# Kernel tuning notes

Hardware: AMD Instinct MI355X
Metric: run time of the kernel (lower is better)

## Reference

```python
import jax, jax.numpy as jnp
import numpy as np

KNN = 10       # knn_size
TOPK = 4       # top_k_select
H = 4          # num_heads
HID = 64       # edge-MLP hidden dim


def setup_inputs() -> dict:
    key = jax.random.key(0)
    ks = jax.random.split(key, 12)
    B, V, D = 4, 4096, 256
    s = 0.02
    return {
        "voxel_tokens": jax.random.normal(ks[0], (B, V, D), jnp.float32),
        "voxel_coords": jax.random.uniform(ks[1], (B, V, 3), jnp.float32) * 10.0,
        "mask": jnp.ones((B, V), dtype=bool),
        # EdgeScoringMLP: Linear(2D+3 -> 64), Linear(64 -> 1)
        "W1": jax.random.normal(ks[2], (2 * D + 3, HID), jnp.float32) * s,
        "b1": jnp.zeros((HID,), jnp.float32),
        "W2": jax.random.normal(ks[3], (HID, 1), jnp.float32) * s,
        "b2": jnp.zeros((1,), jnp.float32),
        # CrossAttention projections (D -> D)
        "Wq": jax.random.normal(ks[4], (D, D), jnp.float32) * s,
        "bq": jnp.zeros((D,), jnp.float32),
        "Wk": jax.random.normal(ks[5], (D, D), jnp.float32) * s,
        "bk": jnp.zeros((D,), jnp.float32),
        "Wv": jax.random.normal(ks[6], (D, D), jnp.float32) * s,
        "bv": jnp.zeros((D,), jnp.float32),
        "Wo": jax.random.normal(ks[7], (D, D), jnp.float32) * s,
        "bo": jnp.zeros((D,), jnp.float32),
    }


def reference(voxel_tokens, voxel_coords, mask,
              W1, b1, W2, b2, Wq, bq, Wk, bk, Wv, bv, Wo, bo):
    # mask is all-True (Vp == V per batch element), so the original per-batch
    # loop over dynamic voxel counts is an exact vmap over B. Dropouts are in
    # eval mode (identity).
    D = voxel_tokens.shape[-1]
    Dh = D // H

    def single(tok, coo):  # tok: (V, D), coo: (V, 3)
        # --- KNN graph build (squared euclidean; monotonic in true cdist) ---
        sq = jnp.sum(coo * coo, axis=-1)                        # (V,)
        d2 = sq[:, None] + sq[None, :] - 2.0 * (coo @ coo.T)    # (V, V)
        _, knn = jax.lax.top_k(-d2, KNN + 1)                    # smallest dists
        knn = knn[:, 1:]                                        # drop self, (V, KNN)

        # --- edge features: [anchor_tok, neighbor_tok, rel_pos] ---
        nb_tok = tok[knn]                                       # (V, KNN, D)
        rel = coo[knn] - coo[:, None, :]                        # (V, KNN, 3)
        anchor = jnp.broadcast_to(tok[:, None, :], nb_tok.shape)
        ef = jnp.concatenate([anchor, nb_tok, rel], axis=-1)    # (V, KNN, 2D+3)

        # --- edge-MLP scoring + softmax + top-k edge select ---
        sc = (jax.nn.relu(ef @ W1 + b1) @ W2 + b2)[..., 0]      # (V, KNN)
        aw = jax.nn.softmax(sc, axis=-1)
        _, loc = jax.lax.top_k(aw, TOPK)                        # (V, TOPK)
        sel = jnp.take_along_axis(knn, loc, axis=-1)            # (V, TOPK)
        nbr = tok[sel]                                          # (V, TOPK, D)

        # --- cross attention over selected neighbors ---
        Q = (tok @ Wq + bq).reshape(-1, H, Dh)                  # (V, H, Dh)
        K = (nbr @ Wk + bk).reshape(-1, TOPK, H, Dh)            # (V, TOPK, H, Dh)
        Vv = (nbr @ Wv + bv).reshape(-1, TOPK, H, Dh)
        att = jnp.einsum('vhd,vshd->vhs', Q, K) / jnp.sqrt(jnp.float32(Dh))
        w = jax.nn.softmax(att, axis=-1)                        # (V, H, TOPK)
        out = jnp.einsum('vhs,vshd->vhd', w, Vv).reshape(-1, D)
        return out @ Wo + bo                                    # (V, D)

    return jax.vmap(single)(voxel_tokens, voxel_coords)        # (B, V, D)
```

## Files before the change

### kernel.cpp

```cpp
#include <hip/hip_runtime.h>
#include <hip/hip_bf16.h>

#define VV 4096
#define DDIM 256
#define KNN_K 10
#define TK 4

__device__ __forceinline__ float f_sq3(float x, float y, float z) {
    return __fadd_rn(__fadd_rn(__fmul_rn(x, x), __fmul_rn(y, y)), __fmul_rn(z, z));
}
__device__ __forceinline__ float f_dot3(float ax, float ay, float az,
                                        float bx, float by, float bz) {
    float d = __fmul_rn(ax, bx);
    d = __fmaf_rn(ay, by, d);
    d = __fmaf_rn(az, bz, d);
    return d;
}

__device__ __forceinline__ unsigned long long mkkey(float d2, int j) {
    unsigned u = __float_as_uint(d2);
    u ^= (unsigned)((int)u >> 31) | 0x80000000u;
    return ((unsigned long long)u << 32) | (unsigned)j;
}

__device__ __forceinline__ void fma44(const float4 a, const float4 b, float (&c)[4][4]) {
    c[0][0] = fmaf(a.x, b.x, c[0][0]); c[0][1] = fmaf(a.x, b.y, c[0][1]);
    c[0][2] = fmaf(a.x, b.z, c[0][2]); c[0][3] = fmaf(a.x, b.w, c[0][3]);
    c[1][0] = fmaf(a.y, b.x, c[1][0]); c[1][1] = fmaf(a.y, b.y, c[1][1]);
    c[1][2] = fmaf(a.y, b.z, c[1][2]); c[1][3] = fmaf(a.y, b.w, c[1][3]);
    c[2][0] = fmaf(a.z, b.x, c[2][0]); c[2][1] = fmaf(a.z, b.y, c[2][1]);
    c[2][2] = fmaf(a.z, b.z, c[2][2]); c[2][3] = fmaf(a.z, b.w, c[2][3]);
    c[3][0] = fmaf(a.w, b.x, c[3][0]); c[3][1] = fmaf(a.w, b.y, c[3][1]);
    c[3][2] = fmaf(a.w, b.z, c[3][2]); c[3][3] = fmaf(a.w, b.w, c[3][3]);
}

__global__ void __launch_bounds__(256) an_gemm_kernel(
    const float* __restrict__ tok,
    const float* __restrict__ W1,
    const float* __restrict__ coords,
    float* __restrict__ AN,
    float4* __restrict__ cxyzs)
{
    __shared__ float As[16][68];
    __shared__ float Bs[16][68];

    const int mBlock = blockIdx.x * 64;
    const int grp    = blockIdx.y;
    const float* W   = W1 + (size_t)grp * 256 * 64;

    const int tid = threadIdx.x;

    if (grp == 0 && tid < 64) {
        int m = mBlock + tid;
        float x = coords[m * 3 + 0], y = coords[m * 3 + 1], z = coords[m * 3 + 2];
        cxyzs[m] = make_float4(x, y, z, f_sq3(x, y, z));
    }

    const int tx = tid & 15;
    const int ty = tid >> 4;

    const int ar  = tid >> 2;
    const int ac4 = tid & 3;
    const int br  = tid >> 4;
    const int bc4 = tid & 15;

    float acc[4][4] = {};

    for (int k0 = 0; k0 < 256; k0 += 16) {
        float4 a4 = *(const float4*)&tok[(size_t)(mBlock + ar) * 256 + k0 + ac4 * 4];
        As[ac4 * 4 + 0][ar] = a4.x;
        As[ac4 * 4 + 1][ar] = a4.y;
        As[ac4 * 4 + 2][ar] = a4.z;
        As[ac4 * 4 + 3][ar] = a4.w;
        float4 b4 = *(const float4*)&W[(size_t)(k0 + br) * 64 + bc4 * 4];
        *(float4*)&Bs[br][bc4 * 4] = b4;
        __syncthreads();
        #pragma unroll
        for (int kk = 0; kk < 16; kk++) {
            float4 av = *(const float4*)&As[kk][ty * 4];
            float4 bv4 = *(const float4*)&Bs[kk][tx * 4];
            fma44(av, bv4, acc);
        }
        __syncthreads();
    }

    #pragma unroll
    for (int i = 0; i < 4; i++) {
        int m = mBlock + ty * 4 + i;
        float4 o;
        o.x = acc[i][0]; o.y = acc[i][1]; o.z = acc[i][2]; o.w = acc[i][3];
        *(float4*)&AN[(size_t)m * 128 + grp * 64 + tx * 4] = o;
    }
}

__global__ void __launch_bounds__(256) knn_score_kernel(
    const float* __restrict__ AN,
    const float4* __restrict__ cxyzs,
    const float* __restrict__ W1,
    const float* __restrict__ b1,
    const float* __restrict__ W2,
    int* __restrict__ sel)
{
    const int tid  = threadIdx.x;
    const int lane = tid & 63;
    const int wave = tid >> 6;
    const int q    = blockIdx.x * 4 + wave;
    const int base = q & ~4095;
    const int v    = q & 4095;
    const float4* cx = cxyzs + base;

    __shared__ int   sKnn[4][KNN_K];
    __shared__ float sSc[4][KNN_K];
    __shared__ float sHid[4][KNN_K][65];

    float4 cq = cx[v];
    const float qx = cq.x, qy = cq.y, qz = cq.z, sqq = cq.w;

    unsigned long long best   = ~0ull;
    unsigned long long second = ~0ull;
    unsigned long long used   = 0ull;

    #pragma unroll 4
    for (int i = 0; i < 64; i++) {
        int j = i * 64 + lane;
        float4 c = cx[j];
        float dt  = f_dot3(qx, qy, qz, c.x, c.y, c.z);
        float d2v = __fsub_rn(__fadd_rn(sqq, c.w), __fmul_rn(2.0f, dt));
        unsigned long long k = mkkey(d2v, j);
        if (k < best) { second = best; best = k; }
        else if (k < second) { second = k; }
    }

    #pragma unroll 1
    for (int it = 0; it < 11; it++) {
        unsigned long long rb = best;
        #pragma unroll
        for (int off = 1; off < 64; off <<= 1) {
            unsigned olo = __shfl_xor((unsigned)rb, off);
            unsigned ohi = __shfl_xor((unsigned)(rb >> 32), off);
            unsigned long long o = ((unsigned long long)ohi << 32) | olo;
            if (o < rb) rb = o;
        }
        int wj = (int)((unsigned)rb & 4095u);
        if (it >= 1 && lane == 0) sKnn[wave][it - 1] = wj;

        if ((unsigned)best == (unsigned)rb) {
            used |= 1ull << (wj >> 6);
            best = second;
            second = ~0ull;
            if (best == ~0ull) {
                #pragma unroll 1
                for (int i = 0; i < 64; i++) {
                    if ((used >> i) & 1ull) continue;
                    int j = i * 64 + lane;
                    float4 c = cx[j];
                    float dt  = f_dot3(qx, qy, qz, c.x, c.y, c.z);
                    float d2v = __fsub_rn(__fadd_rn(sqq, c.w), __fmul_rn(2.0f, dt));
                    unsigned long long k = mkkey(d2v, j);
                    if (k < best) { second = best; best = k; }
                    else if (k < second) { second = k; }
                }
            }
        }
    }

    const float sAl = AN[(size_t)q * 128 + lane];
    const float b1l = b1[lane];
    const float wr0 = W1[(512 + 0) * 64 + lane];
    const float wr1 = W1[(512 + 1) * 64 + lane];
    const float wr2 = W1[(512 + 2) * 64 + lane];

    #pragma unroll 1
    for (int nb = 0; nb < KNN_K; nb++) {
        int kn = sKnn[wave][nb];
        float4 cn = cx[kn];
        float acc = __fadd_rn(sAl, AN[(size_t)(base + kn) * 128 + 64 + lane]);
        float rel0 = __fsub_rn(cn.x, qx);
        acc = __fmaf_rn(rel0, wr0, acc);
        float rel1 = __fsub_rn(cn.y, qy);
        acc = __fmaf_rn(rel1, wr1, acc);
        float rel2 = __fsub_rn(cn.z, qz);
        acc = __fmaf_rn(rel2, wr2, acc);
        float hid = __fadd_rn(acc, b1l);
        sHid[wave][nb][lane] = hid > 0.0f ? hid : 0.0f;
    }

    if (lane < KNN_K) {
        float s = 0.0f;
        #pragma unroll 8
        for (int h = 0; h < 64; h++)
            s = __fmaf_rn(sHid[wave][lane][h], W2[h], s);
        sSc[wave][lane] = s;
    }

    if (lane == 0) {
        unsigned um = 0;
        #pragma unroll
        for (int s = 0; s < TK; s++) {
            float bests = -3.4e38f; int bj = 0;
            for (int jj = 0; jj < KNN_K; jj++) {
                if (um & (1u << jj)) continue;
                float sc = sSc[wave][jj];
                if (sc > bests) { bests = sc; bj = jj; }
            }
            um |= 1u << bj;
            sel[(size_t)q * TK + s] = base + sKnn[wave][bj];
        }
    }
}

__global__ void __launch_bounds__(256, 1) qkv_gemm_kernel(
    const float* __restrict__ tok,
    const float* __restrict__ Wq, const float* __restrict__ bq,
    const float* __restrict__ Wk, const float* __restrict__ bk,
    const float* __restrict__ Wv, const float* __restrict__ bv,
    float* __restrict__ qkv)
{
    __shared__ float As[16][132];
    __shared__ float Bs[16][132];

    const int mBlock = blockIdx.x * 128;
    const int nb     = blockIdx.y;
    const int grp    = nb >> 1;
    const int nIn    = (nb & 1) * 128;
    const float* W    = (grp == 0) ? Wq : (grp == 1) ? Wk : Wv;
    const float* bias = (grp == 0) ? bq : (grp == 1) ? bk : bv;

    const int tid = threadIdx.x;
    const int tx = tid & 15;
    const int ty = tid >> 4;
    const int ar  = tid >> 2;
    const int ac4 = tid & 3;
    const int br  = tid >> 4;
    const int bc4 = tid & 15;

    float acc00[4][4] = {}, acc01[4][4] = {}, acc10[4][4] = {}, acc11[4][4] = {};

    for (int k0 = 0; k0 < 256; k0 += 16) {
        float4 a0 = *(const float4*)&tok[(size_t)(mBlock + ar) * 256 + k0 + ac4 * 4];
        float4 a1 = *(const float4*)&tok[(size_t)(mBlock + 64 + ar) * 256 + k0 + ac4 * 4];
        As[ac4 * 4 + 0][ar] = a0.x;      As[ac4 * 4 + 0][64 + ar] = a1.x;
        As[ac4 * 4 + 1][ar] = a0.y;      As[ac4 * 4 + 1][64 + ar] = a1.y;
        As[ac4 * 4 + 2][ar] = a0.z;      As[ac4 * 4 + 2][64 + ar] = a1.z;
        As[ac4 * 4 + 3][ar] = a0.w;      As[ac4 * 4 + 3][64 + ar] = a1.w;
        float4 b0 = *(const float4*)&W[(size_t)(k0 + br) * 256 + nIn + bc4 * 4];
        float4 b1v = *(const float4*)&W[(size_t)(k0 + br) * 256 + nIn + 64 + bc4 * 4];
        *(float4*)&Bs[br][bc4 * 4] = b0;
        *(float4*)&Bs[br][64 + bc4 * 4] = b1v;
        __syncthreads();
        #pragma unroll
        for (int kk = 0; kk < 16; kk++) {
            float4 av0 = *(const float4*)&As[kk][ty * 4];
            float4 av1 = *(const float4*)&As[kk][64 + ty * 4];
            float4 bv0 = *(const float4*)&Bs[kk][tx * 4];
            float4 bv1 = *(const float4*)&Bs[kk][64 + tx * 4];
            fma44(av0, bv0, acc00);
            fma44(av0, bv1, acc01);
            fma44(av1, bv0, acc10);
            fma44(av1, bv1, acc11);
        }
        __syncthreads();
    }

    #pragma unroll
    for (int i = 0; i < 4; i++) {
        int m0 = mBlock + ty * 4 + i;
        int m1 = m0 + 64;
        int c0 = nIn + tx * 4;
        int c1 = c0 + 64;
        float4 o;
        o.x = acc00[i][0] + bias[c0 + 0]; o.y = acc00[i][1] + bias[c0 + 1];
        o.z = acc00[i][2] + bias[c0 + 2]; o.w = acc00[i][3] + bias[c0 + 3];
        *(float4*)&qkv[(size_t)m0 * 768 + grp * 256 + c0] = o;
        o.x = acc01[i][0] + bias[c1 + 0]; o.y = acc01[i][1] + bias[c1 + 1];
        o.z = acc01[i][2] + bias[c1 + 2]; o.w = acc01[i][3] + bias[c1 + 3];
        *(float4*)&qkv[(size_t)m0 * 768 + grp * 256 + c1] = o;
        o.x = acc10[i][0] + bias[c0 + 0]; o.y = acc10[i][1] + bias[c0 + 1];
        o.z = acc10[i][2] + bias[c0 + 2]; o.w = acc10[i][3] + bias[c0 + 3];
        *(float4*)&qkv[(size_t)m1 * 768 + grp * 256 + c0] = o;
        o.x = acc11[i][0] + bias[c1 + 0]; o.y = acc11[i][1] + bias[c1 + 1];
        o.z = acc11[i][2] + bias[c1 + 2]; o.w = acc11[i][3] + bias[c1 + 3];
        *(float4*)&qkv[(size_t)m1 * 768 + grp * 256 + c1] = o;
    }
}

__global__ void __launch_bounds__(256) attn_gather_kernel(
    const float* __restrict__ qkv, const int* __restrict__ sel,
    float* __restrict__ attnout)
{
    const int tid  = threadIdx.x;
    const int lane = tid & 63;
    const int wave = tid >> 6;
    const int q    = blockIdx.x * 4 + wave;

    int rows[TK];
    #pragma unroll
    for (int s = 0; s < TK; s++) rows[s] = sel[(size_t)q * TK + s];

    const float* qrow = qkv + (size_t)q * 768;

    #pragma unroll
    for (int h = 0; h < 4; h++) {
        const int d = h * 64 + lane;
        const float qv = qrow[d];

        float att[TK];
        #pragma unroll
        for (int s = 0; s < TK; s++) {
            float p = qv * qkv[(size_t)rows[s] * 768 + 256 + d];
            #pragma unroll
            for (int m = 1; m < 64; m <<= 1) p += __shfl_xor(p, m);
            att[s] = p * 0.125f;
        }

        float mx  = fmaxf(fmaxf(att[0], att[1]), fmaxf(att[2], att[3]));
        float e0 = expf(att[0] - mx), e1 = expf(att[1] - mx),
              e2 = expf(att[2] - mx), e3 = expf(att[3] - mx);
        float inv = 1.0f / (e0 + e1 + e2 + e3);

        float o = (e0 * qkv[(size_t)rows[0] * 768 + 512 + d] +
                   e1 * qkv[(size_t)rows[1] * 768 + 512 + d] +
                   e2 * qkv[(size_t)rows[2] * 768 + 512 + d] +
                   e3 * qkv[(size_t)rows[3] * 768 + 512 + d]) * inv;

        attnout[(size_t)q * 256 + d] = o;
    }
}

__global__ void __launch_bounds__(256, 1) wo_gemm_kernel(
    const float* __restrict__ A,
    const float* __restrict__ Wo, const float* __restrict__ bo,
    float* __restrict__ out)
{
    __shared__ float As[16][132];
    __shared__ float Bs[16][132];

    const int mBlock = blockIdx.x * 128;
    const int nBlock = blockIdx.y * 128;

    const int tid = threadIdx.x;
    const int tx = tid & 15;
    const int ty = tid >> 4;
    const int ar  = tid >> 2;
    const int ac4 = tid & 3;
    const int br  = tid >> 4;
    const int bc4 = tid & 15;

    float acc00[4][4] = {}, acc01[4][4] = {}, acc10[4][4] = {}, acc11[4][4] = {};

    for (int k0 = 0; k0 < 256; k0 += 16) {
        float4 a0 = *(const float4*)&A[(size_t)(mBlock + ar) * 256 + k0 + ac4 * 4];
        float4 a1 = *(const float4*)&A[(size_t)(mBlock + 64 + ar) * 256 + k0 + ac4 * 4];
        As[ac4 * 4 + 0][ar] = a0.x;      As[ac4 * 4 + 0][64 + ar] = a1.x;
        As[ac4 * 4 + 1][ar] = a0.y;      As[ac4 * 4 + 1][64 + ar] = a1.y;
        As[ac4 * 4 + 2][ar] = a0.z;      As[ac4 * 4 + 2][64 + ar] = a1.z;
        As[ac4 * 4 + 3][ar] = a0.w;      As[ac4 * 4 + 3][64 + ar] = a1.w;
        float4 b0 = *(const float4*)&Wo[(size_t)(k0 + br) * 256 + nBlock + bc4 * 4];
        float4 b1v = *(const float4*)&Wo[(size_t)(k0 + br) * 256 + nBlock + 64 + bc4 * 4];
        *(float4*)&Bs[br][bc4 * 4] = b0;
        *(float4*)&Bs[br][64 + bc4 * 4] = b1v;
        __syncthreads();
        #pragma unroll
        for (int kk = 0; kk < 16; kk++) {
            float4 av0 = *(const float4*)&As[kk][ty * 4];
            float4 av1 = *(const float4*)&As[kk][64 + ty * 4];
            float4 bv0 = *(const float4*)&Bs[kk][tx * 4];
            float4 bv1 = *(const float4*)&Bs[kk][64 + tx * 4];
            fma44(av0, bv0, acc00);
            fma44(av0, bv1, acc01);
            fma44(av1, bv0, acc10);
            fma44(av1, bv1, acc11);
        }
        __syncthreads();
    }

    #pragma unroll
    for (int i = 0; i < 4; i++) {
        int m0 = mBlock + ty * 4 + i;
        int m1 = m0 + 64;
        int c0 = nBlock + tx * 4;
        int c1 = c0 + 64;
        float4 o;
        o.x = acc00[i][0] + bo[c0 + 0]; o.y = acc00[i][1] + bo[c0 + 1];
        o.z = acc00[i][2] + bo[c0 + 2]; o.w = acc00[i][3] + bo[c0 + 3];
        *(float4*)&out[(size_t)m0 * 256 + c0] = o;
        o.x = acc01[i][0] + bo[c1 + 0]; o.y = acc01[i][1] + bo[c1 + 1];
        o.z = acc01[i][2] + bo[c1 + 2]; o.w = acc01[i][3] + bo[c1 + 3];
        *(float4*)&out[(size_t)m0 * 256 + c1] = o;
        o.x = acc10[i][0] + bo[c0 + 0]; o.y = acc10[i][1] + bo[c0 + 1];
        o.z = acc10[i][2] + bo[c0 + 2]; o.w = acc10[i][3] + bo[c0 + 3];
        *(float4*)&out[(size_t)m1 * 256 + c0] = o;
        o.x = acc11[i][0] + bo[c1 + 0]; o.y = acc11[i][1] + bo[c1 + 1];
        o.z = acc11[i][2] + bo[c1 + 2]; o.w = acc11[i][3] + bo[c1 + 3];
        *(float4*)&out[(size_t)m1 * 256 + c1] = o;
    }
}

__global__ void __launch_bounds__(256) fused_voxel_attn(
    const float* __restrict__ tok,
    const float* __restrict__ coords,
    const float* __restrict__ W1,
    const float* __restrict__ b1,
    const float* __restrict__ W2,
    const float* __restrict__ Wq, const float* __restrict__ bq,
    const float* __restrict__ Wk, const float* __restrict__ bk,
    const float* __restrict__ Wv, const float* __restrict__ bv,
    const float* __restrict__ Wo, const float* __restrict__ bo,
    float* __restrict__ out, int out_size)
{
    const int q    = blockIdx.x;
    const int b    = q >> 12;
    const int v    = q & 4095;
    const int base = q & ~4095;
    const int tid  = threadIdx.x;
    const float* cb = coords + (size_t)b * VV * 3;

    __shared__ float  sval[256];
    __shared__ int    sidx[256];
    __shared__ int    sKnn[KNN_K];
    __shared__ int    sSel[TK];
    __shared__ float  sTokA[DDIM];
    __shared__ float  sTokN[KNN_K][DDIM];
    __shared__ float  sAH[64];
    __shared__ float  sHid[KNN_K][64];
    __shared__ float  sSc[KNN_K];
    __shared__ float  sP[TK][256];
    __shared__ float  sAtt[4][TK];
    __shared__ float  sO[DDIM];

    const float qx = cb[v * 3 + 0];
    const float qy = cb[v * 3 + 1];
    const float qz = cb[v * 3 + 2];
    const float sqq = f_sq3(qx, qy, qz);

    float d2[16];
// ... 57 lines not shown
            acc = __fmaf_rn(tn[k], W1[(256 + k) * 64 + h], acc);
        #pragma unroll
        for (int c = 0; c < 3; c++) {
            float rel = __fsub_rn(cb[sKnn[nb] * 3 + c], cb[v * 3 + c]);
            acc = __fmaf_rn(rel, W1[(512 + c) * 64 + h], acc);
        }
        float hid = __fadd_rn(acc, b1[h]);
        sHid[nb][h] = hid > 0.0f ? hid : 0.0f;
    }
    __syncthreads();

    if (tid < KNN_K) {
        float s = 0.0f;
        for (int h = 0; h < 64; h++)
            s = __fmaf_rn(sHid[tid][h], W2[h], s);
        sSc[tid] = s;
    }
    __syncthreads();

    if (tid == 0) {
        unsigned um = 0;
        #pragma unroll
        for (int s = 0; s < TK; s++) {
            float best = -3.4e38f; int bj = 0;
            for (int jj = 0; jj < KNN_K; jj++) {
                if (um & (1u << jj)) continue;
                if (sSc[jj] > best) { best = sSc[jj]; bj = jj; }
            }
            um |= 1u << bj;
            sSel[s] = bj;
        }
    }
    __syncthreads();

    int ss[TK];
    float k_acc[TK], v_acc[TK];
    #pragma unroll
    for (int s = 0; s < TK; s++) {
        ss[s] = sSel[s];
        k_acc[s] = bk[tid];
        v_acc[s] = bv[tid];
    }
    float q_acc = bq[tid];

    for (int k = 0; k < 256; k++) {
        float wq = Wq[k * 256 + tid];
        float wk = Wk[k * 256 + tid];
        float wv = Wv[k * 256 + tid];
        q_acc += sTokA[k] * wq;
        #pragma unroll
        for (int s = 0; s < TK; s++) {
            float x = sTokN[ss[s]][k];
            k_acc[s] += x * wk;
            v_acc[s] += x * wv;
        }
    }

    #pragma unroll
    for (int s = 0; s < TK; s++) sP[s][tid] = q_acc * k_acc[s];
    __syncthreads();

    if (tid < 16) {
        int h = tid >> 2, s = tid & 3;
        float p = 0.0f;
        for (int d = 0; d < 64; d++) p += sP[s][h * 64 + d];
        sAtt[h][s] = p * 0.125f;
    }
    __syncthreads();

    const int hh = tid >> 6;
    float a0 = sAtt[hh][0], a1 = sAtt[hh][1], a2 = sAtt[hh][2], a3 = sAtt[hh][3];
    float mx  = fmaxf(fmaxf(a0, a1), fmaxf(a2, a3));
    float e0 = expf(a0 - mx), e1 = expf(a1 - mx), e2 = expf(a2 - mx), e3 = expf(a3 - mx);
    float inv = 1.0f / (e0 + e1 + e2 + e3);
    float o = (e0 * v_acc[0] + e1 * v_acc[1] + e2 * v_acc[2] + e3 * v_acc[3]) * inv;

    sO[tid] = o;
    __syncthreads();

    float a = bo[tid];
    for (int e = 0; e < 256; e++) a += sO[e] * Wo[e * 256 + tid];
    int oidx = q * DDIM + tid;
    if (oidx < out_size)
        out[oidx] = a;
}

extern "C" void kernel_launch(void* const* d_in, const int* in_sizes, int n_in,
                              void* d_out, int out_size, void* d_ws, size_t ws_size,
                              hipStream_t stream)
{
    const long long want[13] = {4194304LL, 49152LL, 32960LL, 64LL, 64LL,
                                65536LL, 256LL, 65536LL, 256LL,
                                65536LL, 256LL, 65536LL, 256LL};
    int idx[13];
    const int n = n_in;

    const long long* s64 = (const long long*)(const void*)in_sizes;
    const int*       s32 = in_sizes;

    bool ok = false;

    if (n >= 13 && s64[0] == want[0]) {
        ok = true;
        int walk = 0;
        for (int t = 0; t < 13; t++) {
            int f = -1;
            for (int i = walk; i < n; i++) {
                if (s64[i] == want[t]) { f = i; break; }
            }
            if (f < 0) { ok = false; break; }
            idx[t] = f; walk = f + 1;
        }
    }

    if (!ok) {
        ok = true;
        int walk = 0;
        for (int t = 0; t < 13; t++) {
            int f = -1;
            for (int i = walk; i < n; i++) {
                if ((long long)s32[i] == want[t]) { f = i; break; }
            }
            if (f < 0) { ok = false; break; }
            idx[t] = f; walk = f + 1;
        }
    }

    if (!ok) return;

    const float* tok    = (const float*)d_in[idx[0]];
    const float* coords = (const float*)d_in[idx[1]];
    const float* W1     = (const float*)d_in[idx[2]];
    const float* b1     = (const float*)d_in[idx[3]];
    const float* W2     = (const float*)d_in[idx[4]];
    const float* Wq     = (const float*)d_in[idx[5]];
    const float* bq     = (const float*)d_in[idx[6]];
    const float* Wk     = (const float*)d_in[idx[7]];
    const float* bk     = (const float*)d_in[idx[8]];
    const float* Wv     = (const float*)d_in[idx[9]];
    const float* bv     = (const float*)d_in[idx[10]];
    const float* Wo     = (const float*)d_in[idx[11]];
    const float* bo     = (const float*)d_in[idx[12]];
    float* out = (float*)d_out;

    const size_t NEED = 67633152;
    if (ws_size >= NEED) {
        char* ws = (char*)d_ws;
        int*    sel     = (int*)   (ws + 0);
        float*  AN      = (float*) (ws + 262144);
        float*  attnout = (float*) (ws + 262144);
        float*  qkv     = (float*) (ws + 17039360);
        float4* cxyzs   = (float4*)(ws + 67371008);

        an_gemm_kernel<<<dim3(256, 2), dim3(256), 0, stream>>>(tok, W1, coords, AN, cxyzs);
        knn_score_kernel<<<dim3(4096), dim3(256), 0, stream>>>(AN, cxyzs, W1, b1, W2, sel);
        qkv_gemm_kernel<<<dim3(128, 6), dim3(256), 0, stream>>>(tok, Wq, bq, Wk, bk, Wv, bv, qkv);
        attn_gather_kernel<<<dim3(4096), dim3(256), 0, stream>>>(qkv, sel, attnout);
        wo_gemm_kernel<<<dim3(128, 2), dim3(256), 0, stream>>>(attnout, Wo, bo, out);
    } else {
        fused_voxel_attn<<<dim3(16384), dim3(256), 0, stream>>>(
            tok, coords, W1, b1, W2, Wq, bq, Wk, bk, Wv, bv, Wo, bo, out, out_size);
    }
}
```

Baseline: 367.2 us.

## Fuse KNN scoring and QKV GEMM into one interleaved launch

New measurement: 376.1 us. 2.4% more time.

```diff
diff --git a/kernel.cpp b/kernel.cpp
--- a/kernel.cpp
+++ b/kernel.cpp
@@ -93,194 +93,199 @@
     }
 }
 
-__global__ void __launch_bounds__(256) knn_score_kernel(
+__global__ void __launch_bounds__(256, 1) knn_qkv_kernel(
     const float* __restrict__ AN,
     const float4* __restrict__ cxyzs,
     const float* __restrict__ W1,
     const float* __restrict__ b1,
     const float* __restrict__ W2,
-    int* __restrict__ sel)
-{
-    const int tid  = threadIdx.x;
-    const int lane = tid & 63;
-    const int wave = tid >> 6;
-    const int q    = blockIdx.x * 4 + wave;
-    const int base = q & ~4095;
-    const int v    = q & 4095;
-    const float4* cx = cxyzs + base;
-
-    __shared__ int   sKnn[4][KNN_K];
-    __shared__ float sSc[4][KNN_K];
-    __shared__ float sHid[4][KNN_K][65];
-
-    float4 cq = cx[v];
-    const float qx = cq.x, qy = cq.y, qz = cq.z, sqq = cq.w;
-
-    unsigned long long best   = ~0ull;
-    unsigned long long second = ~0ull;
-    unsigned long long used   = 0ull;
-
-    #pragma unroll 4
-    for (int i = 0; i < 64; i++) {
-        int j = i * 64 + lane;
-        float4 c = cx[j];
-        float dt  = f_dot3(qx, qy, qz, c.x, c.y, c.z);
-        float d2v = __fsub_rn(__fadd_rn(sqq, c.w), __fmul_rn(2.0f, dt));
-        unsigned long long k = mkkey(d2v, j);
-        if (k < best) { second = best; best = k; }
-        else if (k < second) { second = k; }
-    }
-
-    #pragma unroll 1
-    for (int it = 0; it < 11; it++) {
-        unsigned long long rb = best;
-        #pragma unroll
-        for (int off = 1; off < 64; off <<= 1) {
-            unsigned olo = __shfl_xor((unsigned)rb, off);
-            unsigned ohi = __shfl_xor((unsigned)(rb >> 32), off);
-            unsigned long long o = ((unsigned long long)ohi << 32) | olo;
-            if (o < rb) rb = o;
-        }
-        int wj = (int)((unsigned)rb & 4095u);
-        if (it >= 1 && lane == 0) sKnn[wave][it - 1] = wj;
-
-        if ((unsigned)best == (unsigned)rb) {
-            used |= 1ull << (wj >> 6);
-            best = second;
-            second = ~0ull;
-            if (best == ~0ull) {
-                #pragma unroll 1
-                for (int i = 0; i < 64; i++) {
-                    if ((used >> i) & 1ull) continue;
-                    int j = i * 64 + lane;
-                    float4 c = cx[j];
-                    float dt  = f_dot3(qx, qy, qz, c.x, c.y, c.z);
-                    float d2v = __fsub_rn(__fadd_rn(sqq, c.w), __fmul_rn(2.0f, dt));
-                    unsigned long long k = mkkey(d2v, j);
-                    if (k < best) { second = best; best = k; }
-                    else if (k < second) { second = k; }
-                }
-            }
-        }
-    }
-
-    const float sAl = AN[(size_t)q * 128 + lane];
-    const float b1l = b1[lane];
-    const float wr0 = W1[(512 + 0) * 64 + lane];
-    const float wr1 = W1[(512 + 1) * 64 + lane];
-    const float wr2 = W1[(512 + 2) * 64 + lane];
-
-    #pragma unroll 1
-    for (int nb = 0; nb < KNN_K; nb++) {
-        int kn = sKnn[wave][nb];
-        float4 cn = cx[kn];
-        float acc = __fadd_rn(sAl, AN[(size_t)(base + kn) * 128 + 64 + lane]);
-        float rel0 = __fsub_rn(cn.x, qx);
-        acc = __fmaf_rn(rel0, wr0, acc);
-        float rel1 = __fsub_rn(cn.y, qy);
-        acc = __fmaf_rn(rel1, wr1, acc);
-        float rel2 = __fsub_rn(cn.z, qz);
-        acc = __fmaf_rn(rel2, wr2, acc);
-        float hid = __fadd_rn(acc, b1l);
-        sHid[wave][nb][lane] = hid > 0.0f ? hid : 0.0f;
-    }
-
-    if (lane < KNN_K) {
-        float s = 0.0f;
-        #pragma unroll 8
-        for (int h = 0; h < 64; h++)
-            s = __fmaf_rn(sHid[wave][lane][h], W2[h], s);
-        sSc[wave][lane] = s;
-    }
-
-    if (lane == 0) {
-        unsigned um = 0;
-        #pragma unroll
-        for (int s = 0; s < TK; s++) {
-            float bests = -3.4e38f; int bj = 0;
-            for (int jj = 0; jj < KNN_K; jj++) {
-                if (um & (1u << jj)) continue;
-                float sc = sSc[wave][jj];
-                if (sc > bests) { bests = sc; bj = jj; }
-            }
-            um |= 1u << bj;
-            sel[(size_t)q * TK + s] = base + sKnn[wave][bj];
-        }
-    }
-}
-
-__global__ void __launch_bounds__(256, 1) qkv_gemm_kernel(
+    int* __restrict__ sel,
     const float* __restrict__ tok,
     const float* __restrict__ Wq, const float* __restrict__ bq,
     const float* __restrict__ Wk, const float* __restrict__ bk,
     const float* __restrict__ Wv, const float* __restrict__ bv,
     float* __restrict__ qkv)
 {
-    __shared__ float As[16][132];
-    __shared__ float Bs[16][132];
-
-    const int mBlock = blockIdx.x * 128;
-    const int nb     = blockIdx.y;
-    const int grp    = nb >> 1;
-    const int nIn    = (nb & 1) * 128;
-    const float* W    = (grp == 0) ? Wq : (grp == 1) ? Wk : Wv;
-    const float* bias = (grp == 0) ? bq : (grp == 1) ? bk : bv;
-
-    const int tid = threadIdx.x;
-    const int tx = tid & 15;
-    const int ty = tid >> 4;
-    const int ar  = tid >> 2;
-    const int ac4 = tid & 3;
-    const int br  = tid >> 4;
-    const int bc4 = tid & 15;
-
-    float acc00[4][4] = {}, acc01[4][4] = {}, acc10[4][4] = {}, acc11[4][4] = {};
-
-    for (int k0 = 0; k0 < 256; k0 += 16) {
-        float4 a0 = *(const float4*)&tok[(size_t)(mBlock + ar) * 256 + k0 + ac4 * 4];
-        float4 a1 = *(const float4*)&tok[(size_t)(mBlock + 64 + ar) * 256 + k0 + ac4 * 4];
-        As[ac4 * 4 + 0][ar] = a0.x;      As[ac4 * 4 + 0][64 + ar] = a1.x;
-        As[ac4 * 4 + 1][ar] = a0.y;      As[ac4 * 4 + 1][64 + ar] = a1.y;
-        As[ac4 * 4 + 2][ar] = a0.z;      As[ac4 * 4 + 2][64 + ar] = a1.z;
-        As[ac4 * 4 + 3][ar] = a0.w;      As[ac4 * 4 + 3][64 + ar] = a1.w;
-        float4 b0 = *(const float4*)&W[(size_t)(k0 + br) * 256 + nIn + bc4 * 4];
-        float4 b1v = *(const float4*)&W[(size_t)(k0 + br) * 256 + nIn + 64 + bc4 * 4];
-        *(float4*)&Bs[br][bc4 * 4] = b0;
-        *(float4*)&Bs[br][64 + bc4 * 4] = b1v;
-        __syncthreads();
-        #pragma unroll
-        for (int kk = 0; kk < 16; kk++) {
-            float4 av0 = *(const float4*)&As[kk][ty * 4];
-            float4 av1 = *(const float4*)&As[kk][64 + ty * 4];
-            float4 bv0 = *(const float4*)&Bs[kk][tx * 4];
-            float4 bv1 = *(const float4*)&Bs[kk][64 + tx * 4];
-            fma44(av0, bv0, acc00);
-            fma44(av0, bv1, acc01);
-            fma44(av1, bv0, acc10);
-            fma44(av1, bv1, acc11);
-        }
-        __syncthreads();
-    }
-
-    #pragma unroll
-    for (int i = 0; i < 4; i++) {
-        int m0 = mBlock + ty * 4 + i;
-        int m1 = m0 + 64;
-        int c0 = nIn + tx * 4;
-        int c1 = c0 + 64;
-        float4 o;
-        o.x = acc00[i][0] + bias[c0 + 0]; o.y = acc00[i][1] + bias[c0 + 1];
-        o.z = acc00[i][2] + bias[c0 + 2]; o.w = acc00[i][3] + bias[c0 + 3];
-        *(float4*)&qkv[(size_t)m0 * 768 + grp * 256 + c0] = o;
-        o.x = acc01[i][0] + bias[c1 + 0]; o.y = acc01[i][1] + bias[c1 + 1];
-        o.z = acc01[i][2] + bias[c1 + 2]; o.w = acc01[i][3] + bias[c1 + 3];
-        *(float4*)&qkv[(size_t)m0 * 768 + grp * 256 + c1] = o;
-        o.x = acc10[i][0] + bias[c0 + 0]; o.y = acc10[i][1] + bias[c0 + 1];
-        o.z = acc10[i][2] + bias[c0 + 2]; o.w = acc10[i][3] + bias[c0 + 3];
-        *(float4*)&qkv[(size_t)m1 * 768 + grp * 256 + c0] = o;
-        o.x = acc11[i][0] + bias[c1 + 0]; o.y = acc11[i][1] + bias[c1 + 1];
-        o.z = acc11[i][2] + bias[c1 + 2]; o.w = acc11[i][3] + bias[c1 + 3];
-        *(float4*)&qkv[(size_t)m1 * 768 + grp * 256 + c1] = o;
+    __shared__ __align__(16) char smem[16896];
+    const int tid   = threadIdx.x;
+    const int g     = blockIdx.x;
+    const int group = g / 19;
+    const int rem   = g - group * 19;
+
+    if (rem < 16) {
+        const int kb   = group * 16 + rem;
+        const int lane = tid & 63;
+        const int wave = tid >> 6;
+        const int q    = kb * 4 + wave;
+        const int base = q & ~4095;
+        const int v    = q & 4095;
+        const float4* cx = cxyzs + base;
+
+        int*   sKnn = (int*)smem;
+        float* sSc  = (float*)(smem + 160);
+        float* sHid = (float*)(smem + 320);
+
+        float4 cq = cx[v];
+        const float qx = cq.x, qy = cq.y, qz = cq.z, sqq = cq.w;
+
+        unsigned long long best   = ~0ull;
+        unsigned long long second = ~0ull;
+        unsigned long long used   = 0ull;
+
+        #pragma unroll 4
+        for (int i = 0; i < 64; i++) {
+            int j = i * 64 + lane;
+            float4 c = cx[j];
+            float dt  = f_dot3(qx, qy, qz, c.x, c.y, c.z);
+            float d2v = __fsub_rn(__fadd_rn(sqq, c.w), __fmul_rn(2.0f, dt));
+            unsigned long long k = mkkey(d2v, j);
+            if (k < best) { second = best; best = k; }
+            else if (k < second) { second = k; }
+        }
+
+        #pragma unroll 1
+        for (int it = 0; it < 11; it++) {
+            unsigned long long rb = best;
+            #pragma unroll
+            for (int off = 1; off < 64; off <<= 1) {
+                unsigned olo = __shfl_xor((unsigned)rb, off);
+                unsigned ohi = __shfl_xor((unsigned)(rb >> 32), off);
+                unsigned long long o = ((unsigned long long)ohi << 32) | olo;
+                if (o < rb) rb = o;
+            }
+            int wj = (int)((unsigned)rb & 4095u);
+            if (it >= 1 && lane == 0) sKnn[wave * KNN_K + it - 1] = wj;
+
+            if ((unsigned)best == (unsigned)rb) {
+                used |= 1ull << (wj >> 6);
+                best = second;
+                second = ~0ull;
+                if (best == ~0ull) {
+                    #pragma unroll 1
+                    for (int i = 0; i < 64; i++) {
+                        if ((used >> i) & 1ull) continue;
+                        int j = i * 64 + lane;
+                        float4 c = cx[j];
+                        float dt  = f_dot3(qx, qy, qz, c.x, c.y, c.z);
+                        float d2v = __fsub_rn(__fadd_rn(sqq, c.w), __fmul_rn(2.0f, dt));
+                        unsigned long long k = mkkey(d2v, j);
+                        if (k < best) { second = best; best = k; }
+                        else if (k < second) { second = k; }
+                    }
+                }
+            }
+        }
+
+        const float sAl = AN[(size_t)q * 128 + lane];
+        const float b1l = b1[lane];
+        const float wr0 = W1[(512 + 0) * 64 + lane];
+        const float wr1 = W1[(512 + 1) * 64 + lane];
+        const float wr2 = W1[(512 + 2) * 64 + lane];
+
+        #pragma unroll 1
+        for (int nb = 0; nb < KNN_K; nb++) {
+            int kn = sKnn[wave * KNN_K + nb];
+            float4 cn = cx[kn];
+            float acc = __fadd_rn(sAl, AN[(size_t)(base + kn) * 128 + 64 + lane]);
+            float rel0 = __fsub_rn(cn.x, qx);
+            acc = __fmaf_rn(rel0, wr0, acc);
+            float rel1 = __fsub_rn(cn.y, qy);
+            acc = __fmaf_rn(rel1, wr1, acc);
+            float rel2 = __fsub_rn(cn.z, qz);
+            acc = __fmaf_rn(rel2, wr2, acc);
+            float hid = __fadd_rn(acc, b1l);
+            sHid[(wave * KNN_K + nb) * 65 + lane] = hid > 0.0f ? hid : 0.0f;
+        }
+
+        if (lane < KNN_K) {
+            float s = 0.0f;
+            #pragma unroll 8
+            for (int h = 0; h < 64; h++)
+                s = __fmaf_rn(sHid[(wave * KNN_K + lane) * 65 + h], W2[h], s);
+            sSc[wave * KNN_K + lane] = s;
+        }
+
+        if (lane == 0) {
+            unsigned um = 0;
+            #pragma unroll
+            for (int s = 0; s < TK; s++) {
+                float bests = -3.4e38f; int bj = 0;
+                for (int jj = 0; jj < KNN_K; jj++) {
+                    if (um & (1u << jj)) continue;
+                    float sc = sSc[wave * KNN_K + jj];
+                    if (sc > bests) { bests = sc; bj = jj; }
+                }
+                um |= 1u << bj;
+                sel[(size_t)q * TK + s] = base + sKnn[wave * KNN_K + bj];
+            }
+        }
+    } else {
+        float* As = (float*)smem;
+        float* Bs = (float*)smem + 16 * 132;
+
+        const int id     = group * 3 + (rem - 16);
+        const int mBlock = (id & 127) * 128;
+        const int nb     = id >> 7;
+        const int grp    = nb >> 1;
+        const int nIn    = (nb & 1) * 128;
+        const float* W    = (grp == 0) ? Wq : (grp == 1) ? Wk : Wv;
+        const float* bias = (grp == 0) ? bq : (grp == 1) ? bk : bv;
+
+        const int tx = tid & 15;
+        const int ty = tid >> 4;
+        const int ar  = tid >> 2;
+        const int ac4 = tid & 3;
+        const int br  = tid >> 4;
+        const int bc4 = tid & 15;
+
+        float acc00[4][4] = {}, acc01[4][4] = {}, acc10[4][4] = {}, acc11[4][4] = {};
+
+        for (int k0 = 0; k0 < 256; k0 += 16) {
+            float4 a0 = *(const float4*)&tok[(size_t)(mBlock + ar) * 256 + k0 + ac4 * 4];
+            float4 a1 = *(const float4*)&tok[(size_t)(mBlock + 64 + ar) * 256 + k0 + ac4 * 4];
+            As[(ac4 * 4 + 0) * 132 + ar] = a0.x;      As[(ac4 * 4 + 0) * 132 + 64 + ar] = a1.x;
+            As[(ac4 * 4 + 1) * 132 + ar] = a0.y;      As[(ac4 * 4 + 1) * 132 + 64 + ar] = a1.y;
+            As[(ac4 * 4 + 2) * 132 + ar] = a0.z;      As[(ac4 * 4 + 2) * 132 + 64 + ar] = a1.z;
+            As[(ac4 * 4 + 3) * 132 + ar] = a0.w;      As[(ac4 * 4 + 3) * 132 + 64 + ar] = a1.w;
+            float4 b0 = *(const float4*)&W[(size_t)(k0 + br) * 256 + nIn + bc4 * 4];
+            float4 b1v = *(const float4*)&W[(size_t)(k0 + br) * 256 + nIn + 64 + bc4 * 4];
+            *(float4*)&Bs[br * 132 + bc4 * 4] = b0;
+            *(float4*)&Bs[br * 132 + 64 + bc4 * 4] = b1v;
+            __syncthreads();
+            #pragma unroll
+            for (int kk = 0; kk < 16; kk++) {
+                float4 av0 = *(const float4*)&As[kk * 132 + ty * 4];
+                float4 av1 = *(const float4*)&As[kk * 132 + 64 + ty * 4];
+                float4 bv0 = *(const float4*)&Bs[kk * 132 + tx * 4];
+                float4 bv1 = *(const float4*)&Bs[kk * 132 + 64 + tx * 4];
+                fma44(av0, bv0, acc00);
+                fma44(av0, bv1, acc01);
+                fma44(av1, bv0, acc10);
+                fma44(av1, bv1, acc11);
+            }
+            __syncthreads();
+        }
+
+        #pragma unroll
+        for (int i = 0; i < 4; i++) {
+            int m0 = mBlock + ty * 4 + i;
+            int m1 = m0 + 64;
+            int c0 = nIn + tx * 4;
+            int c1 = c0 + 64;
+            float4 o;
+            o.x = acc00[i][0] + bias[c0 + 0]; o.y = acc00[i][1] + bias[c0 + 1];
+            o.z = acc00[i][2] + bias[c0 + 2]; o.w = acc00[i][3] + bias[c0 + 3];
+            *(float4*)&qkv[(size_t)m0 * 768 + grp * 256 + c0] = o;
+            o.x = acc01[i][0] + bias[c1 + 0]; o.y = acc01[i][1] + bias[c1 + 1];
+            o.z = acc01[i][2] + bias[c1 + 2]; o.w = acc01[i][3] + bias[c1 + 3];
+            *(float4*)&qkv[(size_t)m0 * 768 + grp * 256 + c1] = o;
+            o.x = acc10[i][0] + bias[c0 + 0]; o.y = acc10[i][1] + bias[c0 + 1];
+            o.z = acc10[i][2] + bias[c0 + 2]; o.w = acc10[i][3] + bias[c0 + 3];
+            *(float4*)&qkv[(size_t)m1 * 768 + grp * 256 + c0] = o;
+            o.x = acc11[i][0] + bias[c1 + 0]; o.y = acc11[i][1] + bias[c1 + 1];
+            o.z = acc11[i][2] + bias[c1 + 2]; o.w = acc11[i][3] + bias[c1 + 3];
+            *(float4*)&qkv[(size_t)m1 * 768 + grp * 256 + c1] = o;
+        }
     }
 }
 
@@ -645,8 +650,8 @@
         float4* cxyzs   = (float4*)(ws + 67371008);
 
         an_gemm_kernel<<<dim3(256, 2), dim3(256), 0, stream>>>(tok, W1, coords, AN, cxyzs);
-        knn_score_kernel<<<dim3(4096), dim3(256), 0, stream>>>(AN, cxyzs, W1, b1, W2, sel);
-        qkv_gemm_kernel<<<dim3(128, 6), dim3(256), 0, stream>>>(tok, Wq, bq, Wk, bk, Wv, bv, qkv);
+        knn_qkv_kernel<<<dim3(4864), dim3(256), 0, stream>>>(
+            AN, cxyzs, W1, b1, W2, sel, tok, Wq, bq, Wk, bk, Wv, bv, qkv);
         attn_gather_kernel<<<dim3(4096), dim3(256), 0, stream>>>(qkv, sel, attnout);
         wo_gemm_kernel<<<dim3(128, 2), dim3(256), 0, stream>>>(attnout, Wo, bo, out);
     } else {
```

## Merge QKV and edge-MLP GEMMs into one launch; process two queries per wave in KNN

Applied to the files above, without the earlier changes.

Result: slower. 431.3 us (+17.5%).

```diff
diff --git a/kernel.cpp b/kernel.cpp
--- a/kernel.cpp
+++ b/kernel.cpp
@@ -34,62 +34,114 @@
     c[3][2] = fmaf(a.w, b.z, c[3][2]); c[3][3] = fmaf(a.w, b.w, c[3][3]);
 }
 
-__global__ void __launch_bounds__(256) an_gemm_kernel(
+__global__ void __launch_bounds__(256, 1) qkv_an_gemm_kernel(
     const float* __restrict__ tok,
+    const float* __restrict__ Wq, const float* __restrict__ bq,
+    const float* __restrict__ Wk, const float* __restrict__ bk,
+    const float* __restrict__ Wv, const float* __restrict__ bv,
     const float* __restrict__ W1,
     const float* __restrict__ coords,
+    float* __restrict__ qkv,
     float* __restrict__ AN,
     float4* __restrict__ cxyzs)
 {
-    __shared__ float As[16][68];
-    __shared__ float Bs[16][68];
-
-    const int mBlock = blockIdx.x * 64;
-    const int grp    = blockIdx.y;
-    const float* W   = W1 + (size_t)grp * 256 * 64;
-
-    const int tid = threadIdx.x;
-
-    if (grp == 0 && tid < 64) {
+    __shared__ float As[16][132];
+    __shared__ float Bs[16][132];
+
+    const int mBlock = blockIdx.x * 128;
+    const int nb     = blockIdx.y;
+    const int tid    = threadIdx.x;
+
+    if (nb == 6 && tid < 128) {
         int m = mBlock + tid;
         float x = coords[m * 3 + 0], y = coords[m * 3 + 1], z = coords[m * 3 + 2];
         cxyzs[m] = make_float4(x, y, z, f_sq3(x, y, z));
     }
 
+    const int grp    = nb >> 1;
+    const int nIn    = (nb & 1) * 128;
+    const float* W    = (grp == 0) ? Wq : (grp == 1) ? Wk : Wv;
+    const float* bias = (grp == 0) ? bq : (grp == 1) ? bk : bv;
+
     const int tx = tid & 15;
     const int ty = tid >> 4;
-
     const int ar  = tid >> 2;
     const int ac4 = tid & 3;
     const int br  = tid >> 4;
     const int bc4 = tid & 15;
 
-    float acc[4][4] = {};
+    float acc00[4][4] = {}, acc01[4][4] = {}, acc10[4][4] = {}, acc11[4][4] = {};
 
     for (int k0 = 0; k0 < 256; k0 += 16) {
-        float4 a4 = *(const float4*)&tok[(size_t)(mBlock + ar) * 256 + k0 + ac4 * 4];
-        As[ac4 * 4 + 0][ar] = a4.x;
-        As[ac4 * 4 + 1][ar] = a4.y;
-        As[ac4 * 4 + 2][ar] = a4.z;
-        As[ac4 * 4 + 3][ar] = a4.w;
-        float4 b4 = *(const float4*)&W[(size_t)(k0 + br) * 64 + bc4 * 4];
-        *(float4*)&Bs[br][bc4 * 4] = b4;
+        float4 a0 = *(const float4*)&tok[(size_t)(mBlock + ar) * 256 + k0 + ac4 * 4];
+        float4 a1 = *(const float4*)&tok[(size_t)(mBlock + 64 + ar) * 256 + k0 + ac4 * 4];
+        As[ac4 * 4 + 0][ar] = a0.x;      As[ac4 * 4 + 0][64 + ar] = a1.x;
+        As[ac4 * 4 + 1][ar] = a0.y;      As[ac4 * 4 + 1][64 + ar] = a1.y;
+        As[ac4 * 4 + 2][ar] = a0.z;      As[ac4 * 4 + 2][64 + ar] = a1.z;
+        As[ac4 * 4 + 3][ar] = a0.w;      As[ac4 * 4 + 3][64 + ar] = a1.w;
+        float4 b0, b1v;
+        if (nb < 6) {
+            b0  = *(const float4*)&W[(size_t)(k0 + br) * 256 + nIn + bc4 * 4];
+            b1v = *(const float4*)&W[(size_t)(k0 + br) * 256 + nIn + 64 + bc4 * 4];
+        } else {
+            b0  = *(const float4*)&W1[(size_t)(k0 + br) * 64 + bc4 * 4];
+            b1v = *(const float4*)&W1[(size_t)(256 + k0 + br) * 64 + bc4 * 4];
+        }
+        *(float4*)&Bs[br][bc4 * 4] = b0;
+        *(float4*)&Bs[br][64 + bc4 * 4] = b1v;
         __syncthreads();
         #pragma unroll
         for (int kk = 0; kk < 16; kk++) {
-            float4 av = *(const float4*)&As[kk][ty * 4];
-            float4 bv4 = *(const float4*)&Bs[kk][tx * 4];
-            fma44(av, bv4, acc);
+            float4 av0 = *(const float4*)&As[kk][ty * 4];
+            float4 av1 = *(const float4*)&As[kk][64 + ty * 4];
+            float4 bv0 = *(const float4*)&Bs[kk][tx * 4];
+            float4 bv1 = *(const float4*)&Bs[kk][64 + tx * 4];
+            fma44(av0, bv0, acc00);
+            fma44(av0, bv1, acc01);
+            fma44(av1, bv0, acc10);
+            fma44(av1, bv1, acc11);
         }
         __syncthreads();
     }
 
-    #pragma unroll
-    for (int i = 0; i < 4; i++) {
-        int m = mBlock + ty * 4 + i;
-        float4 o;
-        o.x = acc[i][0]; o.y = acc[i][1]; o.z = acc[i][2]; o.w = acc[i][3];
-        *(float4*)&AN[(size_t)m * 128 + grp * 64 + tx * 4] = o;
+    if (nb < 6) {
+        #pragma unroll
+        for (int i = 0; i < 4; i++) {
+            int m0 = mBlock + ty * 4 + i;
+            int m1 = m0 + 64;
+            int c0 = nIn + tx * 4;
+            int c1 = c0 + 64;
+            float4 o;
+            o.x = acc00[i][0] + bias[c0 + 0]; o.y = acc00[i][1] + bias[c0 + 1];
+            o.z = acc00[i][2] + bias[c0 + 2]; o.w = acc00[i][3] + bias[c0 + 3];
+            *(float4*)&qkv[(size_t)m0 * 768 + grp * 256 + c0] = o;
+            o.x = acc01[i][0] + bias[c1 + 0]; o.y = acc01[i][1] + bias[c1 + 1];
+            o.z = acc01[i][2] + bias[c1 + 2]; o.w = acc01[i][3] + bias[c1 + 3];
+            *(float4*)&qkv[(size_t)m0 * 768 + grp * 256 + c1] = o;
+            o.x = acc10[i][0] + bias[c0 + 0]; o.y = acc10[i][1] + bias[c0 + 1];
+            o.z = acc10[i][2] + bias[c0 + 2]; o.w = acc10[i][3] + bias[c0 + 3];
+            *(float4*)&qkv[(size_t)m1 * 768 + grp * 256 + c0] = o;
+            o.x = acc11[i][0] + bias[c1 + 0]; o.y = acc11[i][1] + bias[c1 + 1];
+            o.z = acc11[i][2] + bias[c1 + 2]; o.w = acc11[i][3] + bias[c1 + 3];
+            *(float4*)&qkv[(size_t)m1 * 768 + grp * 256 + c1] = o;
+        }
+    } else {
+        #pragma unroll
+        for (int i = 0; i < 4; i++) {
+            int m0 = mBlock + ty * 4 + i;
+            int m1 = m0 + 64;
+            int c0 = tx * 4;
+            int c1 = c0 + 64;
+            float4 o;
+            o.x = acc00[i][0]; o.y = acc00[i][1]; o.z = acc00[i][2]; o.w = acc00[i][3];
+            *(float4*)&AN[(size_t)m0 * 128 + c0] = o;
+            o.x = acc01[i][0]; o.y = acc01[i][1]; o.z = acc01[i][2]; o.w = acc01[i][3];
+            *(float4*)&AN[(size_t)m0 * 128 + c1] = o;
+            o.x = acc10[i][0]; o.y = acc10[i][1]; o.z = acc10[i][2]; o.w = acc10[i][3];
+            *(float4*)&AN[(size_t)m1 * 128 + c0] = o;
+            o.x = acc11[i][0]; o.y = acc11[i][1]; o.z = acc11[i][2]; o.w = acc11[i][3];
+            *(float4*)&AN[(size_t)m1 * 128 + c1] = o;
+        }
     }
 }
 
@@ -104,67 +156,96 @@
     const int tid  = threadIdx.x;
     const int lane = tid & 63;
     const int wave = tid >> 6;
-    const int q    = blockIdx.x * 4 + wave;
-    const int base = q & ~4095;
-    const int v    = q & 4095;
+    const int qA   = blockIdx.x * 8 + wave * 2;
+    const int qB   = qA + 1;
+    const int base = qA & ~4095;
     const float4* cx = cxyzs + base;
 
-    __shared__ int   sKnn[4][KNN_K];
-    __shared__ float sSc[4][KNN_K];
-    __shared__ float sHid[4][KNN_K][65];
-
-    float4 cq = cx[v];
-    const float qx = cq.x, qy = cq.y, qz = cq.z, sqq = cq.w;
-
-    unsigned long long best   = ~0ull;
-    unsigned long long second = ~0ull;
-    unsigned long long used   = 0ull;
+    __shared__ int   sKnn[4][2][KNN_K];
+    __shared__ float sSc[4][2][KNN_K];
+    __shared__ float sHid[4][2][KNN_K][65];
+
+    float4 cqA = cx[qA & 4095];
+    float4 cqB = cx[qB & 4095];
+
+    unsigned long long bestA = ~0ull, secondA = ~0ull, usedA = 0ull;
+    unsigned long long bestB = ~0ull, secondB = ~0ull, usedB = 0ull;
 
     #pragma unroll 4
     for (int i = 0; i < 64; i++) {
         int j = i * 64 + lane;
         float4 c = cx[j];
-        float dt  = f_dot3(qx, qy, qz, c.x, c.y, c.z);
-        float d2v = __fsub_rn(__fadd_rn(sqq, c.w), __fmul_rn(2.0f, dt));
-        unsigned long long k = mkkey(d2v, j);
-        if (k < best) { second = best; best = k; }
-        else if (k < second) { second = k; }
+        float dtA = f_dot3(cqA.x, cqA.y, cqA.z, c.x, c.y, c.z);
+        float dA  = __fsub_rn(__fadd_rn(cqA.w, c.w), __fmul_rn(2.0f, dtA));
+        unsigned long long kA = mkkey(dA, j);
+        if (kA < bestA) { secondA = bestA; bestA = kA; }
+        else if (kA < secondA) { secondA = kA; }
+        float dtB = f_dot3(cqB.x, cqB.y, cqB.z, c.x, c.y, c.z);
+        float dB  = __fsub_rn(__fadd_rn(cqB.w, c.w), __fmul_rn(2.0f, dtB));
+        unsigned long long kB = mkkey(dB, j);
+        if (kB < bestB) { secondB = bestB; bestB = kB; }
+        else if (kB < secondB) { secondB = kB; }
     }
 
     #pragma unroll 1
     for (int it = 0; it < 11; it++) {
-        unsigned long long rb = best;
+        unsigned long long rbA = bestA, rbB = bestB;
         #pragma unroll
         for (int off = 1; off < 64; off <<= 1) {
-            unsigned olo = __shfl_xor((unsigned)rb, off);
-            unsigned ohi = __shfl_xor((unsigned)(rb >> 32), off);
-            unsigned long long o = ((unsigned long long)ohi << 32) | olo;
-            if (o < rb) rb = o;
-        }
-        int wj = (int)((unsigned)rb & 4095u);
-        if (it >= 1 && lane == 0) sKnn[wave][it - 1] = wj;
-
-        if ((unsigned)best == (unsigned)rb) {
-            used |= 1ull << (wj >> 6);
-            best = second;
-            second = ~0ull;
-            if (best == ~0ull) {
+            unsigned aLo = __shfl_xor((unsigned)rbA, off);
+            unsigned aHi = __shfl_xor((unsigned)(rbA >> 32), off);
+            unsigned bLo = __shfl_xor((unsigned)rbB, off);
+            unsigned bHi = __shfl_xor((unsigned)(rbB >> 32), off);
+            unsigned long long oA = ((unsigned long long)aHi << 32) | aLo;
+            unsigned long long oB = ((unsigned long long)bHi << 32) | bLo;
+            if (oA < rbA) rbA = oA;
+            if (oB < rbB) rbB = oB;
+        }
+        int wjA = (int)((unsigned)rbA & 4095u);
+        int wjB = (int)((unsigned)rbB & 4095u);
+        if (it >= 1 && lane == 0) {
+            sKnn[wave][0][it - 1] = wjA;
+            sKnn[wave][1][it - 1] = wjB;
+        }
+
+        if ((unsigned)bestA == (unsigned)rbA) {
+            usedA |= 1ull << (wjA >> 6);
+            bestA = secondA; secondA = ~0ull;
+            if (bestA == ~0ull) {
                 #pragma unroll 1
                 for (int i = 0; i < 64; i++) {
-                    if ((used >> i) & 1ull) continue;
+                    if ((usedA >> i) & 1ull) continue;
                     int j = i * 64 + lane;
                     float4 c = cx[j];
-                    float dt  = f_dot3(qx, qy, qz, c.x, c.y, c.z);
-                    float d2v = __fsub_rn(__fadd_rn(sqq, c.w), __fmul_rn(2.0f, dt));
-                    unsigned long long k = mkkey(d2v, j);
-                    if (k < best) { second = best; best = k; }
-                    else if (k < second) { second = k; }
+                    float dt = f_dot3(cqA.x, cqA.y, cqA.z, c.x, c.y, c.z);
+                    float d  = __fsub_rn(__fadd_rn(cqA.w, c.w), __fmul_rn(2.0f, dt));
+                    unsigned long long k = mkkey(d, j);
+                    if (k < bestA) { secondA = bestA; bestA = k; }
+                    else if (k < secondA) { secondA = k; }
                 }
             }
         }
-    }
-
-    const float sAl = AN[(size_t)q * 128 + lane];
+        if ((unsigned)bestB == (unsigned)rbB) {
+            usedB |= 1ull << (wjB >> 6);
+            bestB = secondB; secondB = ~0ull;
+            if (bestB == ~0ull) {
+                #pragma unroll 1
+                for (int i = 0; i < 64; i++) {
+                    if ((usedB >> i) & 1ull) continue;
+                    int j = i * 64 + lane;
+                    float4 c = cx[j];
+                    float dt = f_dot3(cqB.x, cqB.y, cqB.z, c.x, c.y, c.z);
+                    float d  = __fsub_rn(__fadd_rn(cqB.w, c.w), __fmul_rn(2.0f, dt));
+                    unsigned long long k = mkkey(d, j);
+                    if (k < bestB) { secondB = bestB; bestB = k; }
+                    else if (k < secondB) { secondB = k; }
+                }
+            }
+        }
+    }
+
+    const float sAlA = AN[(size_t)qA * 128 + lane];
+    const float sAlB = AN[(size_t)qB * 128 + lane];
     const float b1l = b1[lane];
     const float wr0 = W1[(512 + 0) * 64 + lane];
     const float wr1 = W1[(512 + 1) * 64 + lane];
@@ -172,115 +253,52 @@
 
     #pragma unroll 1
     for (int nb = 0; nb < KNN_K; nb++) {
-        int kn = sKnn[wave][nb];
-        float4 cn = cx[kn];
-        float acc = __fadd_rn(sAl, AN[(size_t)(base + kn) * 128 + 64 + lane]);
-        float rel0 = __fsub_rn(cn.x, qx);
-        acc = __fmaf_rn(rel0, wr0, acc);
-        float rel1 = __fsub_rn(cn.y, qy);
-        acc = __fmaf_rn(rel1, wr1, acc);
-        float rel2 = __fsub_rn(cn.z, qz);
-        acc = __fmaf_rn(rel2, wr2, acc);
-        float hid = __fadd_rn(acc, b1l);
-        sHid[wave][nb][lane] = hid > 0.0f ? hid : 0.0f;
-    }
-
-    if (lane < KNN_K) {
-        float s = 0.0f;
-        #pragma unroll 8
-        for (int h = 0; h < 64; h++)
-            s = __fmaf_rn(sHid[wave][lane][h], W2[h], s);
-        sSc[wave][lane] = s;
-    }
-
-    if (lane == 0) {
+        int knA = sKnn[wave][0][nb];
+        int knB = sKnn[wave][1][nb];
+        float4 cnA = cx[knA];
+        float4 cnB = cx[knB];
+        float accA = __fadd_rn(sAlA, AN[(size_t)(base + knA) * 128 + 64 + lane]);
+        float accB = __fadd_rn(sAlB, AN[(size_t)(base + knB) * 128 + 64 + lane]);
+        accA = __fmaf_rn(__fsub_rn(cnA.x, cqA.x), wr0, accA);
+        accB = __fmaf_rn(__fsub_rn(cnB.x, cqB.x), wr0, accB);
+        accA = __fmaf_rn(__fsub_rn(cnA.y, cqA.y), wr1, accA);
+        accB = __fmaf_rn(__fsub_rn(cnB.y, cqB.y), wr1, accB);
+        accA = __fmaf_rn(__fsub_rn(cnA.z, cqA.z), wr2, accA);
+        accB = __fmaf_rn(__fsub_rn(cnB.z, cqB.z), wr2, accB);
+        float hidA = __fadd_rn(accA, b1l);
+        float hidB = __fadd_rn(accB, b1l);
+        sHid[wave][0][nb][lane] = hidA > 0.0f ? hidA : 0.0f;
+        sHid[wave][1][nb][lane] = hidB > 0.0f ? hidB : 0.0f;
+    }
+
+    {
+        int sqi = -1, row = 0;
+        if (lane < KNN_K)                        { sqi = 0; row = lane; }
+        else if (lane >= 32 && lane < 32 + KNN_K) { sqi = 1; row = lane - 32; }
+        if (sqi >= 0) {
+            float s = 0.0f;
+            #pragma unroll 8
+            for (int h = 0; h < 64; h++)
+                s = __fmaf_rn(sHid[wave][sqi][row][h], W2[h], s);
+            sSc[wave][sqi][row] = s;
+        }
+    }
+
+    if (lane == 0 || lane == 32) {
+        const int sqi = lane >> 5;
+        const int qq  = sqi == 0 ? qA : qB;
         unsigned um = 0;
         #pragma unroll
         for (int s = 0; s < TK; s++) {
             float bests = -3.4e38f; int bj = 0;
             for (int jj = 0; jj < KNN_K; jj++) {
                 if (um & (1u << jj)) continue;
-                float sc = sSc[wave][jj];
+                float sc = sSc[wave][sqi][jj];
                 if (sc > bests) { bests = sc; bj = jj; }
             }
             um |= 1u << bj;
-            sel[(size_t)q * TK + s] = base + sKnn[wave][bj];
-        }
-    }
-}
-
-__global__ void __launch_bounds__(256, 1) qkv_gemm_kernel(
-    const float* __restrict__ tok,
-    const float* __restrict__ Wq, const float* __restrict__ bq,
-    const float* __restrict__ Wk, const float* __restrict__ bk,
-    const float* __restrict__ Wv, const float* __restrict__ bv,
-    float* __restrict__ qkv)
-{
-    __shared__ float As[16][132];
-    __shared__ float Bs[16][132];
-
-    const int mBlock = blockIdx.x * 128;
-    const int nb     = blockIdx.y;
-    const int grp    = nb >> 1;
-    const int nIn    = (nb & 1) * 128;
-    const float* W    = (grp == 0) ? Wq : (grp == 1) ? Wk : Wv;
-    const float* bias = (grp == 0) ? bq : (grp == 1) ? bk : bv;
-
-    const int tid = threadIdx.x;
-    const int tx = tid & 15;
-    const int ty = tid >> 4;
-    const int ar  = tid >> 2;
-    const int ac4 = tid & 3;
-    const int br  = tid >> 4;
-    const int bc4 = tid & 15;
-
-    float acc00[4][4] = {}, acc01[4][4] = {}, acc10[4][4] = {}, acc11[4][4] = {};
-
-    for (int k0 = 0; k0 < 256; k0 += 16) {
-        float4 a0 = *(const float4*)&tok[(size_t)(mBlock + ar) * 256 + k0 + ac4 * 4];
-        float4 a1 = *(const float4*)&tok[(size_t)(mBlock + 64 + ar) * 256 + k0 + ac4 * 4];
-        As[ac4 * 4 + 0][ar] = a0.x;      As[ac4 * 4 + 0][64 + ar] = a1.x;
-        As[ac4 * 4 + 1][ar] = a0.y;      As[ac4 * 4 + 1][64 + ar] = a1.y;
-        As[ac4 * 4 + 2][ar] = a0.z;      As[ac4 * 4 + 2][64 + ar] = a1.z;
-        As[ac4 * 4 + 3][ar] = a0.w;      As[ac4 * 4 + 3][64 + ar] = a1.w;
-        float4 b0 = *(const float4*)&W[(size_t)(k0 + br) * 256 + nIn + bc4 * 4];
-        float4 b1v = *(const float4*)&W[(size_t)(k0 + br) * 256 + nIn + 64 + bc4 * 4];
-        *(float4*)&Bs[br][bc4 * 4] = b0;
-        *(float4*)&Bs[br][64 + bc4 * 4] = b1v;
-        __syncthreads();
-        #pragma unroll
-        for (int kk = 0; kk < 16; kk++) {
-            float4 av0 = *(const float4*)&As[kk][ty * 4];
-            float4 av1 = *(const float4*)&As[kk][64 + ty * 4];
-            float4 bv0 = *(const float4*)&Bs[kk][tx * 4];
-            float4 bv1 = *(const float4*)&Bs[kk][64 + tx * 4];
-            fma44(av0, bv0, acc00);
-            fma44(av0, bv1, acc01);
-            fma44(av1, bv0, acc10);
-            fma44(av1, bv1, acc11);
-        }
-        __syncthreads();
-    }
-
-    #pragma unroll
-    for (int i = 0; i < 4; i++) {
-        int m0 = mBlock + ty * 4 + i;
-        int m1 = m0 + 64;
-        int c0 = nIn + tx * 4;
-        int c1 = c0 + 64;
-        float4 o;
-        o.x = acc00[i][0] + bias[c0 + 0]; o.y = acc00[i][1] + bias[c0 + 1];
-        o.z = acc00[i][2] + bias[c0 + 2]; o.w = acc00[i][3] + bias[c0 + 3];
-        *(float4*)&qkv[(size_t)m0 * 768 + grp * 256 + c0] = o;
-        o.x = acc01[i][0] + bias[c1 + 0]; o.y = acc01[i][1] + bias[c1 + 1];
-        o.z = acc01[i][2] + bias[c1 + 2]; o.w = acc01[i][3] + bias[c1 + 3];
-        *(float4*)&qkv[(size_t)m0 * 768 + grp * 256 + c1] = o;
-        o.x = acc10[i][0] + bias[c0 + 0]; o.y = acc10[i][1] + bias[c0 + 1];
-        o.z = acc10[i][2] + bias[c0 + 2]; o.w = acc10[i][3] + bias[c0 + 3];
-        *(float4*)&qkv[(size_t)m1 * 768 + grp * 256 + c0] = o;
-        o.x = acc11[i][0] + bias[c1 + 0]; o.y = acc11[i][1] + bias[c1 + 1];
-        o.z = acc11[i][2] + bias[c1 + 2]; o.w = acc11[i][3] + bias[c1 + 3];
-        *(float4*)&qkv[(size_t)m1 * 768 + grp * 256 + c1] = o;
+            sel[(size_t)qq * TK + s] = base + sKnn[wave][sqi][bj];
+        }
     }
 }
 
@@ -644,9 +662,9 @@
         float*  qkv     = (float*) (ws + 17039360);
         float4* cxyzs   = (float4*)(ws + 67371008);
 
-        an_gemm_kernel<<<dim3(256, 2), dim3(256), 0, stream>>>(tok, W1, coords, AN, cxyzs);
-        knn_score_kernel<<<dim3(4096), dim3(256), 0, stream>>>(AN, cxyzs, W1, b1, W2, sel);
-        qkv_gemm_kernel<<<dim3(128, 6), dim3(256), 0, stream>>>(tok, Wq, bq, Wk, bk, Wv, bv, qkv);
+        qkv_an_gemm_kernel<<<dim3(128, 7), dim3(256), 0, stream>>>(
+            tok, Wq, bq, Wk, bk, Wv, bv, W1, coords, qkv, AN, cxyzs);
+        knn_score_kernel<<<dim3(2048), dim3(256), 0, stream>>>(AN, cxyzs, W1, b1, W2, sel);
         attn_gather_kernel<<<dim3(4096), dim3(256), 0, stream>>>(qkv, sel, attnout);
         wo_gemm_kernel<<<dim3(128, 2), dim3(256), 0, stream>>>(attnout, Wo, bo, out);
     } else {
```
